# Kernel tuning notes

Measured on AMD Instinct MI355X. Metric: run time of the kernel, lower is better.

Reference implementation:

```python
import jax, jax.numpy as jnp
import numpy as np

NUM_CLASSES = 21
FEAT_DIM = 256
TEMP = 0.1
EPS = 1e-12  # F.normalize default eps


def setup_inputs() -> dict:
    key = jax.random.key(0)
    k1, k2, k3, k4 = jax.random.split(key, 4)
    H = W = 768
    features = jax.random.normal(k1, (1, FEAT_DIM, H, W), dtype=jnp.float32)
    prototypes = jax.random.normal(k2, (NUM_CLASSES, FEAT_DIM), dtype=jnp.float32)
    outputs = jax.random.normal(k3, (1, NUM_CLASSES, H, W), dtype=jnp.float32)
    labels = jax.random.randint(k4, (1, 1, H, W), 0, NUM_CLASSES, dtype=jnp.int32)
    return {"features": features, "prototypes": prototypes, "outputs": outputs, "labels": labels}


def reference(features, prototypes, outputs, labels):
    # features: [1, D, H, W]; prototypes: [C, D]; labels: [1, 1, H, W]
    B, D, H, W = features.shape
    C = prototypes.shape[0]
    # Per-pixel feature vectors [N, D] (batch=1, matching torch's view(D, -1) semantics)
    f = features[0].reshape(D, H * W).T
    # F.normalize(features_cl, p=2, dim=0): unit-normalize each pixel's feature vector
    norm = jnp.linalg.norm(f, axis=1, keepdims=True)
    fn = f / jnp.maximum(norm, EPS)
    lab = labels.reshape(-1)  # [N]
    # Per-class mean of normalized features (scatter-mean); all C classes present
    sums = jax.ops.segment_sum(fn, lab, num_segments=C)  # [C, D]
    counts = jax.ops.segment_sum(jnp.ones(lab.shape, dtype=fn.dtype), lab, num_segments=C)  # [C]
    features_local_mean = sums / jnp.maximum(counts, 1.0)[:, None]
    # Prototype logits + masked contrastive loss over classes 1..C-1
    logits = (features_local_mean @ prototypes.T) / TEMP  # [C, C]
    shifted = logits - jnp.max(logits, axis=1, keepdims=True)
    denom = jnp.sum(jnp.exp(shifted[1:, 1:]), axis=1)  # [C-1]
    numer_log = jnp.diagonal(shifted)[1:]  # shifted[cl, cl] for cl in 1..C-1
    loss = jnp.mean(jnp.log(denom) - numer_log)
    return loss
```

## Files before the change

### kernel.cpp

```cpp
#include <hip/hip_runtime.h>
#include <math.h>

#define FEAT_DIM 256
#define NCLS 21
#define TEMP 0.1f
#define SPX 32
#define NW 4
#define CPW 64
#define TS 33
#define NREP 8

typedef float f32x4 __attribute__((ext_vector_type(4)));
typedef int   i32x4 __attribute__((ext_vector_type(4)));

__global__ __launch_bounds__(256, 2)
void k_fused(const float* __restrict__ feat, const int* __restrict__ lab,
             float* __restrict__ gsum, float* __restrict__ gcnt, int N) {
    __shared__ float s_tile[NW][CPW * TS];
    __shared__ float s_acc[NCLS * FEAT_DIM];
    __shared__ float s_ssp[2][NW][SPX];
    __shared__ float s_ivr[NW][SPX];
    __shared__ alignas(16) unsigned char s_scb[2][SPX];
    __shared__ alignas(16) unsigned char s_prm[2][SPX];

    const int tid = threadIdx.x, lane = tid & 63, w = tid >> 6;
    const int rg = lane >> 3;
    const int pg = lane & 7;
    const int dbase = w * CPW;
    float* tile = s_tile[w];

    for (int i = tid; i < NCLS * FEAT_DIM; i += 256) s_acc[i] = 0.f;
    __syncthreads();

    const int nsub = N / SPX;
    const int per  = nsub / gridDim.x;
    const int i0   = blockIdx.x * per;

    float cntacc = 0.f;
    float4 VA[8], VB[8];
    int labA = 0, labB = 0;

    {
        const size_t ns = (size_t)i0 * SPX;
        if (w == 0) labA = lab[ns + (lane & 31)];
        #pragma unroll
        for (int j = 0; j < 8; ++j)
            VA[j] = *reinterpret_cast<const float4*>(
                feat + (size_t)(dbase + 8 * j + rg) * N + ns + 4 * pg);
    }

    auto body = [&](int it, float4 (&VC)[8], int labc,
                    float4 (&VN)[8], int& labn) {
        const int buf = it & 1;

        if (it + 1 < per) {
            const size_t ns2 = (size_t)(i0 + it + 1) * SPX;
            if (w == 0) labn = lab[ns2 + (lane & 31)];
            #pragma unroll
            for (int j = 0; j < 8; ++j)
                VN[j] = *reinterpret_cast<const float4*>(
                    feat + (size_t)(dbase + 8 * j + rg) * N + ns2 + 4 * pg);
        }

        if (w == 0) {
            const int p = lane & 31;
            int myrank = 0, base = 0;
            #pragma unroll 1
            for (int c = 0; c < NCLS; ++c) {
                const unsigned long long m = __ballot(labc == c) & 0xFFFFFFFFull;
                const int cnt = (int)__popcll(m);
                if (labc == c)
                    myrank = base + (int)__popcll(m & ((1ull << p) - 1ull));
                if (lane == c) cntacc += (float)cnt;
                base += cnt;
            }
            if (lane < 32) {
                s_scb[buf][myrank] = (unsigned char)labc;
                s_prm[buf][myrank] = (unsigned char)p;
            }
        }

        {
            f32x4 ssv = {0.f, 0.f, 0.f, 0.f};
            #pragma unroll
            for (int j = 0; j < 8; ++j) {
                ssv[0] = fmaf(VC[j].x, VC[j].x, ssv[0]);
                ssv[1] = fmaf(VC[j].y, VC[j].y, ssv[1]);
                ssv[2] = fmaf(VC[j].z, VC[j].z, ssv[2]);
                ssv[3] = fmaf(VC[j].w, VC[j].w, ssv[3]);
            }
            #pragma unroll
            for (int e = 0; e < 4; ++e) {
                ssv[e] += __shfl_xor(ssv[e], 8);
                ssv[e] += __shfl_xor(ssv[e], 16);
                ssv[e] += __shfl_xor(ssv[e], 32);
            }
            if (rg == 0)
                *reinterpret_cast<f32x4*>(&s_ssp[buf][w][4 * pg]) = ssv;
        }

        #pragma unroll
        for (int j = 0; j < 8; ++j) {
            float* t = tile + (8 * j + rg) * TS + 4 * pg;
            t[0] = VC[j].x; t[1] = VC[j].y; t[2] = VC[j].z; t[3] = VC[j].w;
        }

        asm volatile("s_waitcnt lgkmcnt(0)" ::: "memory");
        __builtin_amdgcn_s_barrier();

        {
            const int r = lane & 31;
            const int px = s_prm[buf][r];
            const float ss = s_ssp[buf][0][px] + s_ssp[buf][1][px] +
                             s_ssp[buf][2][px] + s_ssp[buf][3][px];
            s_ivr[w][r] = 1.0f / fmaxf(sqrtf(ss), 1e-12f);
        }

        {
            i32x4 pmv[2], scv[2];
            f32x4 vv[8];
            pmv[0] = *reinterpret_cast<const i32x4*>(&s_prm[buf][0]);
            pmv[1] = *reinterpret_cast<const i32x4*>(&s_prm[buf][16]);
            scv[0] = *reinterpret_cast<const i32x4*>(&s_scb[buf][0]);
            scv[1] = *reinterpret_cast<const i32x4*>(&s_scb[buf][16]);
            #pragma unroll
            for (int j = 0; j < 8; ++j)
                vv[j] = *reinterpret_cast<const f32x4*>(&s_ivr[w][4 * j]);

            const float* trow = tile + lane * TS;
            float val[32];
            #pragma unroll
            for (int k = 0; k < 32; ++k) {
                const int px = (pmv[k >> 4][(k >> 2) & 3] >> (8 * (k & 3))) & 255;
                val[k] = trow[px];
            }

            float acc = 0.f;
            int ccur = __builtin_amdgcn_readfirstlane(scv[0][0] & 255);
            #pragma unroll
            for (int k = 0; k < 32; ++k) {
                const int ck = __builtin_amdgcn_readfirstlane(
                    (scv[k >> 4][(k >> 2) & 3] >> (8 * (k & 3))) & 255);
                if (ck != ccur) {
                    s_acc[ccur * FEAT_DIM + dbase + lane] += acc;
                    acc = 0.f; ccur = ck;
                }
                acc = fmaf(val[k], vv[k >> 2][k & 3], acc);
            }
            s_acc[ccur * FEAT_DIM + dbase + lane] += acc;
        }
    };

    for (int it = 0; it < per; it += 2) {
        body(it,     VA, labA, VB, labB);
        body(it + 1, VB, labB, VA, labA);
    }

    __syncthreads();
    {
        float* grep = gsum + (size_t)(blockIdx.x & (NREP - 1)) * (NCLS * FEAT_DIM);
        const int total = NCLS * FEAT_DIM;
        const int off = (blockIdx.x * 37) % total;
        for (int k = tid; k < total; k += 256) {
            int i = k + off; if (i >= total) i -= total;
            const float v = s_acc[i];
            if (v != 0.f) atomicAdd(&grep[i], v);
        }
    }
    if (w == 0 && lane < NCLS) atomicAdd(&gcnt[lane], cntacc);
}

__global__ void k_final(const float* __restrict__ gsum,
                        const float* __restrict__ gcnt,
                        const float* __restrict__ proto,
                        float* __restrict__ out) {
    __shared__ float s_mean[NCLS * 257];
    __shared__ float s_icnt[NCLS];
    __shared__ float s_log[NCLS * NCLS];
    __shared__ float s_term[NCLS];

    if (threadIdx.x < NCLS)
        s_icnt[threadIdx.x] = 1.0f / fmaxf(gcnt[threadIdx.x], 1.0f);
    __syncthreads();

    for (int i = threadIdx.x; i < NCLS * FEAT_DIM; i += blockDim.x) {
        float v = 0.f;
        #pragma unroll
        for (int r = 0; r < NREP; ++r) v += gsum[r * NCLS * FEAT_DIM + i];
        const int c = i / FEAT_DIM, d = i - c * FEAT_DIM;
        s_mean[c * 257 + d] = v * s_icnt[c];
    }
    __syncthreads();

    for (int p = threadIdx.x; p < NCLS * NCLS; p += blockDim.x) {
        const int c = p / NCLS, j = p - c * NCLS;
        float acc = 0.f;
        #pragma unroll 8
        for (int d = 0; d < FEAT_DIM; ++d)
            acc += s_mean[c * 257 + d] * proto[j * FEAT_DIM + d];
        s_log[p] = acc / TEMP;
    }
    __syncthreads();

    if (threadIdx.x >= 1 && threadIdx.x < NCLS) {
        const int c = threadIdx.x;
        float m = -INFINITY;
        for (int j = 0; j < NCLS; ++j) m = fmaxf(m, s_log[c * NCLS + j]);
        float den = 0.f;
        for (int j = 1; j < NCLS; ++j) den += expf(s_log[c * NCLS + j] - m);
        s_term[c] = logf(den) - (s_log[c * NCLS + c] - m);
    }
    __syncthreads();

    if (threadIdx.x == 0) {
        float acc = 0.f;
        for (int c = 1; c < NCLS; ++c) acc += s_term[c];
        out[0] = acc / (float)(NCLS - 1);
    }
}

extern "C" void kernel_launch(void* const* d_in, const int* in_sizes, int n_in,
                              void* d_out, int out_size, void* d_ws, size_t ws_size,
                              hipStream_t stream) {
    const float* feat  = (const float*)d_in[0];
    const float* proto = (const float*)d_in[1];
    const int*   lab   = (const int*)d_in[3];

    const int N = in_sizes[3];

    float* gsum = (float*)d_ws;
    float* gcnt = gsum + NREP * NCLS * FEAT_DIM;

    hipMemsetAsync(gsum, 0,
                   (NREP * NCLS * FEAT_DIM + NCLS) * sizeof(float), stream);

    k_fused<<<512, 256, 0, stream>>>(feat, lab, gsum, gcnt, N);
    k_final<<<1, 256, 0, stream>>>(gsum, gcnt, proto, (float*)d_out);
}
```

Baseline: 203.2 us.

## Split fused kernel into producer/consumer warps with bf16 shared tiles

Restructures the fused segment-sum kernel into 512-thread blocks in which four producer waves load 128-pixel chunks, compute squared norms, sort labels and stage the features as bf16 into a double-buffered shared tile. The other four consumer waves each own one channel and accumulate normalized values per class run. The aim is to overlap global loads with the accumulation and to halve shared-memory footprint and traffic through bf16 packing. In exchange the accumulated features lose precision, occupancy drops to one large block per CU, and the kernel depends on the producers keeping ahead of the consumers.

Result: slower. 365.8 us (+80.0%).

```diff
diff --git a/kernel.cpp b/kernel.cpp
--- a/kernel.cpp
+++ b/kernel.cpp
@@ -4,156 +4,149 @@
 #define FEAT_DIM 256
 #define NCLS 21
 #define TEMP 0.1f
-#define SPX 32
-#define NW 4
-#define CPW 64
-#define TS 33
+#define CPX 128
+#define RS 130
 #define NREP 8
 
 typedef float f32x4 __attribute__((ext_vector_type(4)));
-typedef int   i32x4 __attribute__((ext_vector_type(4)));
-
-__global__ __launch_bounds__(256, 2)
+
+__device__ __forceinline__ unsigned int cvt_pk_bf16(float lo, float hi) {
+    unsigned int r;
+    asm volatile("v_cvt_pk_bf16_f32 %0, %1, %2" : "=v"(r) : "v"(lo), "v"(hi));
+    return r;
+}
+
+__global__ __launch_bounds__(512, 1)
 void k_fused(const float* __restrict__ feat, const int* __restrict__ lab,
              float* __restrict__ gsum, float* __restrict__ gcnt, int N) {
-    __shared__ float s_tile[NW][CPW * TS];
+    __shared__ unsigned short s_tile[2][256 * RS];
+    __shared__ float s_ssp[2][4][CPX];
+    __shared__ float s_ivk[CPX];
+    __shared__ alignas(16) unsigned char s_prm[2][CPX];
+    __shared__ alignas(16) unsigned char s_scb[2][CPX];
     __shared__ float s_acc[NCLS * FEAT_DIM];
-    __shared__ float s_ssp[2][NW][SPX];
-    __shared__ float s_ivr[NW][SPX];
-    __shared__ alignas(16) unsigned char s_scb[2][SPX];
-    __shared__ alignas(16) unsigned char s_prm[2][SPX];
 
     const int tid = threadIdx.x, lane = tid & 63, w = tid >> 6;
-    const int rg = lane >> 3;
-    const int pg = lane & 7;
-    const int dbase = w * CPW;
-    float* tile = s_tile[w];
-
-    for (int i = tid; i < NCLS * FEAT_DIM; i += 256) s_acc[i] = 0.f;
-    __syncthreads();
-
-    const int nsub = N / SPX;
-    const int per  = nsub / gridDim.x;
-    const int i0   = blockIdx.x * per;
+    const bool consumer = (w < 4);
+
+    for (int i = tid; i < NCLS * FEAT_DIM; i += 512) s_acc[i] = 0.f;
+    __syncthreads();
+
+    const int per = (N / CPX) / gridDim.x;
+    const size_t px0 = (size_t)blockIdx.x * (size_t)per * CPX;
 
     float cntacc = 0.f;
-    float4 VA[8], VB[8];
-    int labA = 0, labB = 0;
-
-    {
-        const size_t ns = (size_t)i0 * SPX;
-        if (w == 0) labA = lab[ns + (lane & 31)];
+
+    auto stage = [&](int cc, int b) {
+        const int pw = w - 4;
+        const int half = lane >> 5;
+        const int pq = lane & 31;
+        const size_t po = px0 + (size_t)cc * CPX;
+        const int rbase = pw * 64 + half;
+        const float* fp = feat + (size_t)rbase * N + po + 4 * pq;
+        unsigned short* tp0 = &s_tile[b][rbase * RS + 4 * pq];
+
+        f32x4 ssq = {0.f, 0.f, 0.f, 0.f};
+        #pragma unroll 8
+        for (int i = 0; i < 32; ++i) {
+            const float4 v = *reinterpret_cast<const float4*>(fp + (size_t)(2 * i) * N);
+            ssq[0] = fmaf(v.x, v.x, ssq[0]);
+            ssq[1] = fmaf(v.y, v.y, ssq[1]);
+            ssq[2] = fmaf(v.z, v.z, ssq[2]);
+            ssq[3] = fmaf(v.w, v.w, ssq[3]);
+            unsigned int* tp = reinterpret_cast<unsigned int*>(tp0 + (size_t)(2 * i) * RS);
+            tp[0] = cvt_pk_bf16(v.x, v.y);
+            tp[1] = cvt_pk_bf16(v.z, v.w);
+        }
         #pragma unroll
-        for (int j = 0; j < 8; ++j)
-            VA[j] = *reinterpret_cast<const float4*>(
-                feat + (size_t)(dbase + 8 * j + rg) * N + ns + 4 * pg);
-    }
-
-    auto body = [&](int it, float4 (&VC)[8], int labc,
-                    float4 (&VN)[8], int& labn) {
-        const int buf = it & 1;
-
-        if (it + 1 < per) {
-            const size_t ns2 = (size_t)(i0 + it + 1) * SPX;
-            if (w == 0) labn = lab[ns2 + (lane & 31)];
-            #pragma unroll
-            for (int j = 0; j < 8; ++j)
-                VN[j] = *reinterpret_cast<const float4*>(
-                    feat + (size_t)(dbase + 8 * j + rg) * N + ns2 + 4 * pg);
-        }
-
-        if (w == 0) {
-            const int p = lane & 31;
+        for (int e = 0; e < 4; ++e) ssq[e] += __shfl_xor(ssq[e], 32);
+        if (half == 0)
+            *reinterpret_cast<f32x4*>(&s_ssp[b][pw][4 * pq]) = ssq;
+
+        if (pw < 2) {
+            const int myl = lab[po + pw * 64 + lane];
             int myrank = 0, base = 0;
             #pragma unroll 1
             for (int c = 0; c < NCLS; ++c) {
-                const unsigned long long m = __ballot(labc == c) & 0xFFFFFFFFull;
+                const unsigned long long m = __ballot(myl == c);
                 const int cnt = (int)__popcll(m);
-                if (labc == c)
-                    myrank = base + (int)__popcll(m & ((1ull << p) - 1ull));
+                if (myl == c)
+                    myrank = base + (int)__popcll(m & ((1ull << lane) - 1ull));
                 if (lane == c) cntacc += (float)cnt;
                 base += cnt;
             }
-            if (lane < 32) {
-                s_scb[buf][myrank] = (unsigned char)labc;
-                s_prm[buf][myrank] = (unsigned char)p;
-            }
-        }
-
-        {
-            f32x4 ssv = {0.f, 0.f, 0.f, 0.f};
+            s_prm[b][pw * 64 + myrank] = (unsigned char)(pw * 64 + lane);
+            s_scb[b][pw * 64 + myrank] = (unsigned char)myl;
+        }
+    };
+
+    auto accumulate = [&](int b) {
+        const int chan = tid;
+        const unsigned short* trow = &s_tile[b][chan * RS];
+        const uint4* pmv = reinterpret_cast<const uint4*>(s_prm[b]);
+        const uint4* scv = reinterpret_cast<const uint4*>(s_scb[b]);
+
+        float acc = 0.f;
+        int ccur = __builtin_amdgcn_readfirstlane((int)s_scb[b][0]);
+
+        #pragma unroll 1
+        for (int bb = 0; bb < 8; ++bb) {
+            const uint4 pm = pmv[bb];
+            const uint4 sc = scv[bb];
+            const unsigned int pmw[4] = {pm.x, pm.y, pm.z, pm.w};
+            const unsigned int scw[4] = {sc.x, sc.y, sc.z, sc.w};
+            const f32x4 vv0 = *reinterpret_cast<const f32x4*>(&s_ivk[16 * bb + 0]);
+            const f32x4 vv1 = *reinterpret_cast<const f32x4*>(&s_ivk[16 * bb + 4]);
+            const f32x4 vv2 = *reinterpret_cast<const f32x4*>(&s_ivk[16 * bb + 8]);
+            const f32x4 vv3 = *reinterpret_cast<const f32x4*>(&s_ivk[16 * bb + 12]);
+
+            unsigned short hv[16];
             #pragma unroll
-            for (int j = 0; j < 8; ++j) {
-                ssv[0] = fmaf(VC[j].x, VC[j].x, ssv[0]);
-                ssv[1] = fmaf(VC[j].y, VC[j].y, ssv[1]);
-                ssv[2] = fmaf(VC[j].z, VC[j].z, ssv[2]);
-                ssv[3] = fmaf(VC[j].w, VC[j].w, ssv[3]);
+            for (int k = 0; k < 16; ++k) {
+                const int px = (int)((pmw[k >> 2] >> (8 * (k & 3))) & 255u);
+                hv[k] = trow[px];
             }
             #pragma unroll
-            for (int e = 0; e < 4; ++e) {
-                ssv[e] += __shfl_xor(ssv[e], 8);
-                ssv[e] += __shfl_xor(ssv[e], 16);
-                ssv[e] += __shfl_xor(ssv[e], 32);
+            for (int k = 0; k < 16; ++k) {
+                const int ck = __builtin_amdgcn_readfirstlane(
+                    (int)((scw[k >> 2] >> (8 * (k & 3))) & 255u));
+                if (ck != ccur) {
+                    s_acc[ccur * FEAT_DIM + chan] += acc;
+                    acc = 0.f; ccur = ck;
+                }
+                const float val = __builtin_bit_cast(
+                    float, (unsigned int)hv[k] << 16);
+                const float iv = (k < 4) ? vv0[k & 3] :
+                                 (k < 8) ? vv1[k & 3] :
+                                 (k < 12) ? vv2[k & 3] : vv3[k & 3];
+                acc = fmaf(val, iv, acc);
             }
-            if (rg == 0)
-                *reinterpret_cast<f32x4*>(&s_ssp[buf][w][4 * pg]) = ssv;
-        }
-
-        #pragma unroll
-        for (int j = 0; j < 8; ++j) {
-            float* t = tile + (8 * j + rg) * TS + 4 * pg;
-            t[0] = VC[j].x; t[1] = VC[j].y; t[2] = VC[j].z; t[3] = VC[j].w;
-        }
-
+        }
+        s_acc[ccur * FEAT_DIM + chan] += acc;
+    };
+
+    if (!consumer) stage(0, 0);
+    asm volatile("s_waitcnt lgkmcnt(0)" ::: "memory");
+    __builtin_amdgcn_s_barrier();
+
+    for (int cc = 0; cc < per; ++cc) {
+        const int b = cc & 1;
+        if (consumer && tid < CPX) {
+            const int px = (int)s_prm[b][tid];
+            const float ss = s_ssp[b][0][px] + s_ssp[b][1][px] +
+                             s_ssp[b][2][px] + s_ssp[b][3][px];
+            s_ivk[tid] = 1.0f / fmaxf(sqrtf(ss), 1e-12f);
+        }
         asm volatile("s_waitcnt lgkmcnt(0)" ::: "memory");
         __builtin_amdgcn_s_barrier();
 
-        {
-            const int r = lane & 31;
-            const int px = s_prm[buf][r];
-            const float ss = s_ssp[buf][0][px] + s_ssp[buf][1][px] +
-                             s_ssp[buf][2][px] + s_ssp[buf][3][px];
-            s_ivr[w][r] = 1.0f / fmaxf(sqrtf(ss), 1e-12f);
-        }
-
-        {
-            i32x4 pmv[2], scv[2];
-            f32x4 vv[8];
-            pmv[0] = *reinterpret_cast<const i32x4*>(&s_prm[buf][0]);
-            pmv[1] = *reinterpret_cast<const i32x4*>(&s_prm[buf][16]);
-            scv[0] = *reinterpret_cast<const i32x4*>(&s_scb[buf][0]);
-            scv[1] = *reinterpret_cast<const i32x4*>(&s_scb[buf][16]);
-            #pragma unroll
-            for (int j = 0; j < 8; ++j)
-                vv[j] = *reinterpret_cast<const f32x4*>(&s_ivr[w][4 * j]);
-
-            const float* trow = tile + lane * TS;
-            float val[32];
-            #pragma unroll
-            for (int k = 0; k < 32; ++k) {
-                const int px = (pmv[k >> 4][(k >> 2) & 3] >> (8 * (k & 3))) & 255;
-                val[k] = trow[px];
-            }
-
-            float acc = 0.f;
-            int ccur = __builtin_amdgcn_readfirstlane(scv[0][0] & 255);
-            #pragma unroll
-            for (int k = 0; k < 32; ++k) {
-                const int ck = __builtin_amdgcn_readfirstlane(
-                    (scv[k >> 4][(k >> 2) & 3] >> (8 * (k & 3))) & 255);
-                if (ck != ccur) {
-                    s_acc[ccur * FEAT_DIM + dbase + lane] += acc;
-                    acc = 0.f; ccur = ck;
-                }
-                acc = fmaf(val[k], vv[k >> 2][k & 3], acc);
-            }
-            s_acc[ccur * FEAT_DIM + dbase + lane] += acc;
-        }
-    };
-
-    for (int it = 0; it < per; it += 2) {
-        body(it,     VA, labA, VB, labB);
-        body(it + 1, VB, labB, VA, labA);
+        if (consumer) {
+            accumulate(b);
+        } else if (cc + 1 < per) {
+            stage(cc + 1, b ^ 1);
+        }
+        asm volatile("s_waitcnt lgkmcnt(0)" ::: "memory");
+        __builtin_amdgcn_s_barrier();
     }
 
     __syncthreads();
@@ -161,13 +154,13 @@
         float* grep = gsum + (size_t)(blockIdx.x & (NREP - 1)) * (NCLS * FEAT_DIM);
         const int total = NCLS * FEAT_DIM;
         const int off = (blockIdx.x * 37) % total;
-        for (int k = tid; k < total; k += 256) {
+        for (int k = tid; k < total; k += 512) {
             int i = k + off; if (i >= total) i -= total;
             const float v = s_acc[i];
             if (v != 0.f) atomicAdd(&grep[i], v);
         }
     }
-    if (w == 0 && lane < NCLS) atomicAdd(&gcnt[lane], cntacc);
+    if ((w == 4 || w == 5) && lane < NCLS) atomicAdd(&gcnt[lane], cntacc);
 }
 
 __global__ void k_final(const float* __restrict__ gsum,
@@ -234,6 +227,6 @@
     hipMemsetAsync(gsum, 0,
                    (NREP * NCLS * FEAT_DIM + NCLS) * sizeof(float), stream);
 
-    k_fused<<<512, 256, 0, stream>>>(feat, lab, gsum, gcnt, N);
+    k_fused<<<256, 512, 0, stream>>>(feat, lab, gsum, gcnt, N);
     k_final<<<1, 256, 0, stream>>>(gsum, gcnt, proto, (float*)d_out);
 }
```
